# Kernel optimization log

Measured on AMD Instinct MI355X. Metric: run time of the kernel, lower is better.

## Reference

```python
import jax, jax.numpy as jnp
import numpy as np

NUM_HEADS = 16

def _stablemax3_s(x):
    # 3rd-order Taylor approx of exp(x), Eq 38
    pos = 1.0 + x * (1.0 + 0.5 * x * (1.0 + x / 3.0))
    neg = 1.0 / (1.0 - x * (1.0 - 0.5 * x * (1.0 - x / 3.0)))
    return jnp.where(x >= 0, pos, neg)

def stablemax3(logits, axis=-1):
    logits = logits - jnp.max(logits, axis=axis, keepdims=True)
    s = _stablemax3_s(logits)
    return s / jnp.sum(s, axis=axis, keepdims=True)

def setup_inputs() -> dict:
    key = jax.random.key(0)
    k1, k2, k3 = jax.random.split(key, 3)
    B, S, D = 2, 2048, 1024
    x = jax.random.normal(k1, (B, S, D), dtype=jnp.float32)
    w_qkv = jax.random.normal(k2, (3 * D, D), dtype=jnp.float32) * 0.02
    w_out = jax.random.normal(k3, (D, D), dtype=jnp.float32) * 0.02
    b_out = jnp.zeros((D,), dtype=jnp.float32)
    return {"x": x, "w_qkv": w_qkv, "w_out": w_out, "b_out": b_out}

def reference(x, w_qkv, w_out, b_out):
    B, S, D = x.shape
    H = NUM_HEADS
    hd = D // H
    scale = hd ** (-0.5)
    qkv = x @ w_qkv.T                                  # [B, S, 3D]
    qkv = qkv.reshape(B, S, 3, H, hd)
    qkv = jnp.transpose(qkv, (2, 0, 3, 1, 4))          # [3, B, H, S, hd]
    q, k, v = qkv[0], qkv[1], qkv[2]                   # pos(.) is identity here
    attn = jnp.einsum('bhsd,bhtd->bhst', q, k) * scale # [B, H, S, S]
    attn = stablemax3(attn, axis=-1)
    out = jnp.einsum('bhst,bhtd->bhsd', attn, v)       # [B, H, S, hd]
    out = jnp.transpose(out, (0, 2, 1, 3)).reshape(B, S, D)
    return out @ w_out.T + b_out
```

## Files before the change

### kernel.cpp

```cpp
#include <hip/hip_runtime.h>

typedef _Float16 half8 __attribute__((ext_vector_type(8)));
typedef _Float16 half4 __attribute__((ext_vector_type(4)));
typedef float floatx4 __attribute__((ext_vector_type(4)));

__device__ __forceinline__ void gl_lds16(const _Float16* g, _Float16* l) {
    __builtin_amdgcn_global_load_lds(
        (const __attribute__((address_space(1))) void*)g,
        (__attribute__((address_space(3))) void*)l, 16, 0, 0);
}

__global__ __launch_bounds__(256) void cvt_f32_f16(const floatx4* __restrict__ in,
                                                   half4* __restrict__ out, int n4) {
    int i = blockIdx.x * 256 + threadIdx.x;
    if (i >= n4) return;
    floatx4 v = in[i];
    half4 h;
#pragma unroll
    for (int j = 0; j < 4; ++j) h[j] = (_Float16)v[j];
    out[i] = h;
}

__global__ __launch_bounds__(256) void gemm_qkv(const _Float16* __restrict__ A,
                                                const _Float16* __restrict__ B,
                                                _Float16* __restrict__ qh,
                                                _Float16* __restrict__ kh,
                                                _Float16* __restrict__ vth) {
    const int K = 1024;
    __shared__ _Float16 SH[128 * 68];
    _Float16* As = SH;
    _Float16* Bs = SH + 4096;
    const int t = threadIdx.x;
    const int lane = t & 63, w = t >> 6;
    const int l15 = lane & 15, quad = lane >> 4;
    const int wm = w >> 1, wn = w & 1;
    const int m0 = blockIdx.y * 128, n0 = blockIdx.x * 128;

    floatx4 acc[4][4];
    const floatx4 zf = {0.f, 0.f, 0.f, 0.f};
#pragma unroll
    for (int i = 0; i < 4; ++i)
#pragma unroll
        for (int j = 0; j < 4; ++j) acc[i][j] = zf;

    for (int kt = 0; kt < K; kt += 32) {
        __syncthreads();
#pragma unroll
        for (int it = 0; it < 2; ++it) {
            int cc = it * 256 + t;
            int row = cc >> 2, kc = cc & 3;
            gl_lds16(&A[(size_t)(m0 + row) * K + kt + kc * 8], &As[cc * 8]);
            gl_lds16(&B[(size_t)(n0 + row) * K + kt + kc * 8], &Bs[cc * 8]);
        }
        __syncthreads();
        half8 af[4], bfr[4];
#pragma unroll
        for (int i = 0; i < 4; ++i)
            af[i] = *(const half8*)&As[(wm * 64 + i * 16 + l15) * 32 + quad * 8];
#pragma unroll
        for (int i = 0; i < 4; ++i)
            bfr[i] = *(const half8*)&Bs[(wn * 64 + i * 16 + l15) * 32 + quad * 8];
#pragma unroll
        for (int mi = 0; mi < 4; ++mi)
#pragma unroll
            for (int ni = 0; ni < 4; ++ni)
                acc[mi][ni] = __builtin_amdgcn_mfma_f32_16x16x32_f16(af[mi], bfr[ni],
                                                                     acc[mi][ni], 0, 0, 0);
    }

    const int b = m0 >> 11, s0 = m0 & 2047;
#pragma unroll
    for (int hf = 0; hf < 2; ++hf) {
        __syncthreads();
        if (wn == hf) {
#pragma unroll
            for (int mi = 0; mi < 4; ++mi)
#pragma unroll
                for (int ni = 0; ni < 4; ++ni)
#pragma unroll
                    for (int r = 0; r < 4; ++r)
                        SH[(wm * 64 + mi * 16 + quad * 4 + r) * 68 + ni * 16 + l15] =
                            (_Float16)acc[mi][ni][r];
        }
        __syncthreads();
        const int cbase = n0 + hf * 64;
        if (n0 < 2048) {
            const int hh = (cbase & 1023) >> 6;
            _Float16* dst = (n0 < 1024 ? qh : kh) + (size_t)((b << 4) | hh) * 131072;
#pragma unroll
            for (int it = 0; it < 4; ++it) {
                int cc = it * 256 + t;
                int r = cc >> 3, c8 = cc & 7;
                half4 lo = *(const half4*)&SH[r * 68 + c8 * 8];
                half4 hi = *(const half4*)&SH[r * 68 + c8 * 8 + 4];
                half8 v;
#pragma unroll
                for (int j = 0; j < 4; ++j) { v[j] = lo[j]; v[j + 4] = hi[j]; }
                *(half8*)&dst[(size_t)(s0 + r) * 64 + c8 * 8] = v;
            }
        } else {
            const int hh = (cbase - 2048) >> 6;
            _Float16* dst = vth + (size_t)((b << 4) | hh) * 131072;
#pragma unroll
            for (int it = 0; it < 4; ++it) {
                int cc = it * 256 + t;
                int d = cc >> 4, s8 = cc & 15;
                half8 v;
#pragma unroll
                for (int j = 0; j < 8; ++j) v[j] = SH[(s8 * 8 + j) * 68 + d];
                *(half8*)&dst[(size_t)d * 2048 + s0 + s8 * 8] = v;
            }
        }
    }
}

__global__ __launch_bounds__(256) void gemm_out(const _Float16* __restrict__ A,
                                                const _Float16* __restrict__ B,
                                                float* __restrict__ C,
                                                const float* __restrict__ bias) {
    const int K = 1024, N = 1024;
    __shared__ _Float16 SH[6144];
    _Float16* As = SH;
    _Float16* Bs = SH + 2048;
    const int t = threadIdx.x;
    const int lane = t & 63, w = t >> 6;
    const int l15 = lane & 15, quad = lane >> 4;
    const int wm = w >> 1, wn = w & 1;
    const int m0 = blockIdx.y * 64, n0 = blockIdx.x * 128;

    floatx4 acc[2][4];
    const floatx4 zf = {0.f, 0.f, 0.f, 0.f};
#pragma unroll
    for (int i = 0; i < 2; ++i)
#pragma unroll
        for (int j = 0; j < 4; ++j) acc[i][j] = zf;

    for (int kt = 0; kt < K; kt += 32) {
        __syncthreads();
        {
            int row = t >> 2, kc = t & 3;
            gl_lds16(&A[(size_t)(m0 + row) * K + kt + kc * 8], &As[t * 8]);
        }
#pragma unroll
        for (int it = 0; it < 2; ++it) {
            int cc = it * 256 + t;
            int row = cc >> 2, kc = cc & 3;
            gl_lds16(&B[(size_t)(n0 + row) * K + kt + kc * 8], &Bs[cc * 8]);
        }
        __syncthreads();
        half8 af[2], bfr[4];
#pragma unroll
        for (int i = 0; i < 2; ++i)
            af[i] = *(const half8*)&As[(wm * 32 + i * 16 + l15) * 32 + quad * 8];
#pragma unroll
        for (int i = 0; i < 4; ++i)
            bfr[i] = *(const half8*)&Bs[(wn * 64 + i * 16 + l15) * 32 + quad * 8];
#pragma unroll
        for (int mi = 0; mi < 2; ++mi)
#pragma unroll
            for (int ni = 0; ni < 4; ++ni)
                acc[mi][ni] = __builtin_amdgcn_mfma_f32_16x16x32_f16(af[mi], bfr[ni],
                                                                     acc[mi][ni], 0, 0, 0);
    }

#pragma unroll
    for (int mi = 0; mi < 2; ++mi) {
#pragma unroll
        for (int ni = 0; ni < 4; ++ni) {
            int col = n0 + wn * 64 + ni * 16 + l15;
            float bv = bias[col];
#pragma unroll
            for (int r = 0; r < 4; ++r) {
                int row = m0 + wm * 32 + mi * 16 + quad * 4 + r;
                C[(size_t)row * N + col] = acc[mi][ni][r] + bv;
            }
        }
    }
}

__device__ inline float s3pos(float a) {
    float h = fmaf(a, 0.16666667f, 0.5f);
    h = fmaf(a, h, 1.0f);
    return fmaf(a, h, 1.0f);
}

__global__ __launch_bounds__(256) void attn_kernel(const _Float16* __restrict__ qh,
                                                   const _Float16* __restrict__ kh,
                                                   const _Float16* __restrict__ vth,
                                                   _Float16* __restrict__ out) {
    __shared__ _Float16 SM[2 * 64 * 72];
    _Float16* Ks = SM;
    _Float16* VTs = SM + 64 * 72;

    const int t = threadIdx.x;
    const int lane = t & 63, w = t >> 6;
    const int l15 = lane & 15, quad = lane >> 4;
    const int q0 = blockIdx.x * 128;
    const int bh = blockIdx.y;
    const int b = bh >> 4, h = bh & 15;

    const _Float16* Qp = qh + (size_t)bh * 131072 + q0 * 64;
    const _Float16* Kp = kh + (size_t)bh * 131072;
    const _Float16* VTp = vth + (size_t)bh * 131072;

    const floatx4 zf = {0.f, 0.f, 0.f, 0.f};

    half8 qf[2][2];
#pragma unroll
    for (int nh = 0; nh < 2; ++nh)
#pragma unroll
        for (int kk = 0; kk < 2; ++kk)
            qf[nh][kk] = *(const half8*)&Qp[(w * 32 + nh * 16 + l15) * 64 + kk * 32 + quad * 8];

    float rmax[2] = {-1.0e30f, -1.0e30f};

    for (int kt = 0; kt < 2048; kt += 64) {
        __syncthreads();
#pragma unroll
        for (int it = 0; it < 2; ++it) {
            int cc = it * 256 + t;
            int r = cc >> 3, c8 = cc & 7;
            *(half8*)&Ks[r * 72 + c8 * 8] = *(const half8*)&Kp[kt * 64 + cc * 8];
        }
        __syncthreads();
        floatx4 sa[4][2];
#pragma unroll
        for (int T = 0; T < 4; ++T) { sa[T][0] = zf; sa[T][1] = zf; }
#pragma unroll
        for (int kk = 0; kk < 2; ++kk) {
            half8 kf[4];
#pragma unroll
            for (int T = 0; T < 4; ++T)
                kf[T] = *(const half8*)&Ks[(T * 16 + l15) * 72 + kk * 32 + quad * 8];
#pragma unroll
            for (int T = 0; T < 4; ++T)
#pragma unroll
                for (int nh = 0; nh < 2; ++nh)
                    sa[T][nh] = __builtin_amdgcn_mfma_f32_16x16x32_f16(kf[T], qf[nh][kk],
                                                                      sa[T][nh], 0, 0, 0);
        }
#pragma unroll
        for (int T = 0; T < 4; ++T)
#pragma unroll
            for (int nh = 0; nh < 2; ++nh)
#pragma unroll
                for (int r = 0; r < 4; ++r)
                    rmax[nh] = fmaxf(rmax[nh], sa[T][nh][r]);
    }
#pragma unroll
    for (int nh = 0; nh < 2; ++nh) {
        rmax[nh] = fmaxf(rmax[nh], __shfl_xor(rmax[nh], 16, 64));
        rmax[nh] = fmaxf(rmax[nh], __shfl_xor(rmax[nh], 32, 64));
    }
    const float xm[2] = {-0.125f * rmax[0], -0.125f * rmax[1]};

    float rsum[2] = {0.f, 0.f};
    floatx4 oacc[4][2];
#pragma unroll
    for (int i = 0; i < 4; ++i) { oacc[i][0] = zf; oacc[i][1] = zf; }

    for (int kt = 0; kt < 2048; kt += 64) {
        __syncthreads();
#pragma unroll
        for (int it = 0; it < 2; ++it) {
            int cc = it * 256 + t;
            int r = cc >> 3, c8 = cc & 7;
            *(half8*)&Ks[r * 72 + c8 * 8] = *(const half8*)&Kp[kt * 64 + cc * 8];
            *(half8*)&VTs[r * 72 + c8 * 8] =
                *(const half8*)&VTp[(size_t)r * 2048 + kt + c8 * 8];
        }
        __syncthreads();
        floatx4 sa[4][2];
#pragma unroll
        for (int T = 0; T < 4; ++T) { sa[T][0] = zf; sa[T][1] = zf; }
#pragma unroll
        for (int kk = 0; kk < 2; ++kk) {
            half8 kf[4];
#pragma unroll
            for (int T = 0; T < 4; ++T)
                kf[T] = *(const half8*)&Ks[(T * 16 + l15) * 72 + kk * 32 + quad * 8];
#pragma unroll
            for (int T = 0; T < 4; ++T)
#pragma unroll
                for (int nh = 0; nh < 2; ++nh)
                    sa[T][nh] = __builtin_amdgcn_mfma_f32_16x16x32_f16(kf[T], qf[nh][kk],
                                                                      sa[T][nh], 0, 0, 0);
        }
        float p[2][4][4];
#pragma unroll
        for (int nh = 0; nh < 2; ++nh)
#pragma unroll
            for (int T = 0; T < 4; ++T)
#pragma unroll
                for (int r = 0; r < 4; ++r) {
                    float x = fmaf(sa[T][nh][r], 0.125f, xm[nh]);
                    float pv = __builtin_amdgcn_rcpf(s3pos(fabsf(x)));
                    p[nh][T][r] = pv;
                    rsum[nh] += pv;
                }
#pragma unroll
        for (int c = 0; c < 2; ++c) {
            half8 vf[4];
#pragma unroll
            for (int di = 0; di < 4; ++di) {
                half4 lo = *(const half4*)&VTs[(di * 16 + l15) * 72 + c * 32 + 4 * quad];
                half4 hi = *(const half4*)&VTs[(di * 16 + l15) * 72 + c * 32 + 16 + 4 * quad];
                half8 vv;
#pragma unroll
                for (int j = 0; j < 4; ++j) { vv[j] = lo[j]; vv[j + 4] = hi[j]; }
                vf[di] = vv;
            }
#pragma unroll
            for (int nh = 0; nh < 2; ++nh) {
                half8 pb;
#pragma unroll
                for (int j = 0; j < 8; ++j)
                    pb[j] = (_Float16)p[nh][2 * c + (j >> 2)][j & 3];
#pragma unroll
                for (int di = 0; di < 4; ++di)
                    oacc[di][nh] = __builtin_amdgcn_mfma_f32_16x16x32_f16(vf[di], pb,
                                                                         oacc[di][nh], 0, 0, 0);
            }
        }
    }

#pragma unroll
    for (int nh = 0; nh < 2; ++nh) {
        rsum[nh] += __shfl_xor(rsum[nh], 16, 64);
        rsum[nh] += __shfl_xor(rsum[nh], 32, 64);
    }
    const float inv[2] = {1.0f / rsum[0], 1.0f / rsum[1]};

    __syncthreads();
    _Float16* Os = SM;
#pragma unroll
    for (int di = 0; di < 4; ++di) {
#pragma unroll
        for (int nh = 0; nh < 2; ++nh) {
            half4 hv;
#pragma unroll
            for (int r = 0; r < 4; ++r) hv[r] = (_Float16)(oacc[di][nh][r] * inv[nh]);
            *(half4*)&Os[(w * 32 + nh * 16 + l15) * 72 + di * 16 + quad * 4] = hv;
        }
    }
    __syncthreads();
    _Float16* Op = out + (size_t)(b * 2048 + q0) * 1024 + h * 64;
#pragma unroll
    for (int it = 0; it < 4; ++it) {
        int cc = it * 256 + t;
        int r = cc >> 3, c8 = cc & 7;
        *(half8*)&Op[(size_t)r * 1024 + c8 * 8] = *(const half8*)&Os[r * 72 + c8 * 8];
    }
}

extern "C" void kernel_launch(void* const* d_in, const int* in_sizes, int n_in,
                              void* d_out, int out_size, void* d_ws, size_t ws_size,
                              hipStream_t stream) {
    const float* x_f = (const float*)d_in[0];
    const float* wqkv_f = (const float*)d_in[1];
    const float* wout_f = (const float*)d_in[2];
    const float* bias_f = (const float*)d_in[3];

    char* ws = (char*)d_ws;
    _Float16* xh = (_Float16*)(ws);
    _Float16* aoh = xh;
    _Float16* wqh = (_Float16*)(ws + 8388608);
    _Float16* woh = wqh;
    _Float16* qh = (_Float16*)(ws + 14680064);
    _Float16* kh = (_Float16*)(ws + 23068672);
    _Float16* vth = (_Float16*)(ws + 31457280);

    cvt_f32_f16<<<4096, 256, 0, stream>>>((const floatx4*)x_f, (half4*)xh, 1048576);
    cvt_f32_f16<<<3072, 256, 0, stream>>>((const floatx4*)wqkv_f, (half4*)wqh, 786432);
    gemm_qkv<<<dim3(24, 32), 256, 0, stream>>>(xh, wqh, qh, kh, vth);
    cvt_f32_f16<<<1024, 256, 0, stream>>>((const floatx4*)wout_f, (half4*)woh, 262144);
    attn_kernel<<<dim3(16, 32), 256, 0, stream>>>(qh, kh, vth, aoh);
    gemm_out<<<dim3(8, 64), 256, 0, stream>>>(aoh, woh, (float*)d_out, bias_f);
}
```

Baseline: 218.3 us.

## Double K-tile depth in GEMMs and attention, fuse input conversion kernels

New measurement: 259.2 us. +18.7%, slower.

```diff
diff --git a/kernel.cpp b/kernel.cpp
--- a/kernel.cpp
+++ b/kernel.cpp
@@ -8,6 +8,27 @@
     __builtin_amdgcn_global_load_lds(
         (const __attribute__((address_space(1))) void*)g,
         (__attribute__((address_space(3))) void*)l, 16, 0, 0);
+}
+
+__global__ __launch_bounds__(256) void cvt_xw(const floatx4* __restrict__ x,
+                                              const floatx4* __restrict__ wq,
+                                              half4* __restrict__ xh,
+                                              half4* __restrict__ wqh) {
+    int i = blockIdx.x * 256 + threadIdx.x;
+    floatx4 v;
+    half4 h;
+    if (i < 1048576) {
+        v = x[i];
+#pragma unroll
+        for (int j = 0; j < 4; ++j) h[j] = (_Float16)v[j];
+        xh[i] = h;
+    } else {
+        int j4 = i - 1048576;
+        v = wq[j4];
+#pragma unroll
+        for (int j = 0; j < 4; ++j) h[j] = (_Float16)v[j];
+        wqh[j4] = h;
+    }
 }
 
 __global__ __launch_bounds__(256) void cvt_f32_f16(const floatx4* __restrict__ in,
@@ -27,140 +48,148 @@
                                                 _Float16* __restrict__ kh,
                                                 _Float16* __restrict__ vth) {
     const int K = 1024;
-    __shared__ _Float16 SH[128 * 68];
+    __shared__ _Float16 SH[128 * 128];
+    _Float16* As = SH;
+    _Float16* Bs = SH + 8192;
+    const int t = threadIdx.x;
+    const int lane = t & 63, w = t >> 6;
+    const int l15 = lane & 15, quad = lane >> 4;
+    const int wm = w >> 1, wn = w & 1;
+    const int m0 = blockIdx.y * 128, n0 = blockIdx.x * 128;
+
+    floatx4 acc[4][4];
+    const floatx4 zf = {0.f, 0.f, 0.f, 0.f};
+#pragma unroll
+    for (int i = 0; i < 4; ++i)
+#pragma unroll
+        for (int j = 0; j < 4; ++j) acc[i][j] = zf;
+
+    for (int kt = 0; kt < K; kt += 64) {
+        __syncthreads();
+#pragma unroll
+        for (int it = 0; it < 4; ++it) {
+            int cc = it * 256 + t;
+            int row = cc >> 3, kc = cc & 7;
+            gl_lds16(&A[(size_t)(m0 + row) * K + kt + kc * 8], &As[cc * 8]);
+            gl_lds16(&B[(size_t)(n0 + row) * K + kt + kc * 8], &Bs[cc * 8]);
+        }
+        __syncthreads();
+#pragma unroll
+        for (int kk = 0; kk < 2; ++kk) {
+            half8 af[4], bfr[4];
+#pragma unroll
+            for (int i = 0; i < 4; ++i)
+                af[i] = *(const half8*)&As[(wm * 64 + i * 16 + l15) * 64 + kk * 32 + quad * 8];
+#pragma unroll
+            for (int i = 0; i < 4; ++i)
+                bfr[i] = *(const half8*)&Bs[(wn * 64 + i * 16 + l15) * 64 + kk * 32 + quad * 8];
+#pragma unroll
+            for (int mi = 0; mi < 4; ++mi)
+#pragma unroll
+                for (int ni = 0; ni < 4; ++ni)
+                    acc[mi][ni] = __builtin_amdgcn_mfma_f32_16x16x32_f16(af[mi], bfr[ni],
+                                                                         acc[mi][ni], 0, 0, 0);
+        }
+    }
+
+    const int b = m0 >> 11, s0 = m0 & 2047;
+#pragma unroll
+    for (int hf = 0; hf < 2; ++hf) {
+        __syncthreads();
+        if (wn == hf) {
+#pragma unroll
+            for (int mi = 0; mi < 4; ++mi)
+#pragma unroll
+                for (int ni = 0; ni < 4; ++ni)
+#pragma unroll
+                    for (int r = 0; r < 4; ++r)
+                        SH[(wm * 64 + mi * 16 + quad * 4 + r) * 68 + ni * 16 + l15] =
+                            (_Float16)acc[mi][ni][r];
+        }
+        __syncthreads();
+        const int cbase = n0 + hf * 64;
+        if (n0 < 2048) {
+            const int hh = (cbase & 1023) >> 6;
+            _Float16* dst = (n0 < 1024 ? qh : kh) + (size_t)((b << 4) | hh) * 131072;
+#pragma unroll
+            for (int it = 0; it < 4; ++it) {
+                int cc = it * 256 + t;
+                int r = cc >> 3, c8 = cc & 7;
+                half4 lo = *(const half4*)&SH[r * 68 + c8 * 8];
+                half4 hi = *(const half4*)&SH[r * 68 + c8 * 8 + 4];
+                half8 v;
+#pragma unroll
+                for (int j = 0; j < 4; ++j) { v[j] = lo[j]; v[j + 4] = hi[j]; }
+                *(half8*)&dst[(size_t)(s0 + r) * 64 + c8 * 8] = v;
+            }
+        } else {
+            const int hh = (cbase - 2048) >> 6;
+            _Float16* dst = vth + (size_t)((b << 4) | hh) * 131072;
+#pragma unroll
+            for (int it = 0; it < 4; ++it) {
+                int cc = it * 256 + t;
+                int d = cc >> 4, s8 = cc & 15;
+                half8 v;
+#pragma unroll
+                for (int j = 0; j < 8; ++j) v[j] = SH[(s8 * 8 + j) * 68 + d];
+                *(half8*)&dst[(size_t)d * 2048 + s0 + s8 * 8] = v;
+            }
+        }
+    }
+}
+
+__global__ __launch_bounds__(256) void gemm_out(const _Float16* __restrict__ A,
+                                                const _Float16* __restrict__ B,
+                                                float* __restrict__ C,
+                                                const float* __restrict__ bias) {
+    const int K = 1024, N = 1024;
+    __shared__ _Float16 SH[12288];
     _Float16* As = SH;
     _Float16* Bs = SH + 4096;
     const int t = threadIdx.x;
     const int lane = t & 63, w = t >> 6;
     const int l15 = lane & 15, quad = lane >> 4;
     const int wm = w >> 1, wn = w & 1;
-    const int m0 = blockIdx.y * 128, n0 = blockIdx.x * 128;
-
-    floatx4 acc[4][4];
+    const int m0 = blockIdx.y * 64, n0 = blockIdx.x * 128;
+
+    floatx4 acc[2][4];
     const floatx4 zf = {0.f, 0.f, 0.f, 0.f};
 #pragma unroll
-    for (int i = 0; i < 4; ++i)
+    for (int i = 0; i < 2; ++i)
 #pragma unroll
         for (int j = 0; j < 4; ++j) acc[i][j] = zf;
 
-    for (int kt = 0; kt < K; kt += 32) {
+    for (int kt = 0; kt < K; kt += 64) {
         __syncthreads();
 #pragma unroll
         for (int it = 0; it < 2; ++it) {
             int cc = it * 256 + t;
-            int row = cc >> 2, kc = cc & 3;
+            int row = cc >> 3, kc = cc & 7;
             gl_lds16(&A[(size_t)(m0 + row) * K + kt + kc * 8], &As[cc * 8]);
+        }
+#pragma unroll
+        for (int it = 0; it < 4; ++it) {
+            int cc = it * 256 + t;
+            int row = cc >> 3, kc = cc & 7;
             gl_lds16(&B[(size_t)(n0 + row) * K + kt + kc * 8], &Bs[cc * 8]);
         }
         __syncthreads();
-        half8 af[4], bfr[4];
-#pragma unroll
-        for (int i = 0; i < 4; ++i)
-            af[i] = *(const half8*)&As[(wm * 64 + i * 16 + l15) * 32 + quad * 8];
-#pragma unroll
-        for (int i = 0; i < 4; ++i)
-            bfr[i] = *(const half8*)&Bs[(wn * 64 + i * 16 + l15) * 32 + quad * 8];
-#pragma unroll
-        for (int mi = 0; mi < 4; ++mi)
-#pragma unroll
-            for (int ni = 0; ni < 4; ++ni)
-                acc[mi][ni] = __builtin_amdgcn_mfma_f32_16x16x32_f16(af[mi], bfr[ni],
-                                                                     acc[mi][ni], 0, 0, 0);
-    }
-
-    const int b = m0 >> 11, s0 = m0 & 2047;
-#pragma unroll
-    for (int hf = 0; hf < 2; ++hf) {
-        __syncthreads();
-        if (wn == hf) {
-#pragma unroll
-            for (int mi = 0; mi < 4; ++mi)
+#pragma unroll
+        for (int kk = 0; kk < 2; ++kk) {
+            half8 af[2], bfr[4];
+#pragma unroll
+            for (int i = 0; i < 2; ++i)
+                af[i] = *(const half8*)&As[(wm * 32 + i * 16 + l15) * 64 + kk * 32 + quad * 8];
+#pragma unroll
+            for (int i = 0; i < 4; ++i)
+                bfr[i] = *(const half8*)&Bs[(wn * 64 + i * 16 + l15) * 64 + kk * 32 + quad * 8];
+#pragma unroll
+            for (int mi = 0; mi < 2; ++mi)
 #pragma unroll
                 for (int ni = 0; ni < 4; ++ni)
-#pragma unroll
-                    for (int r = 0; r < 4; ++r)
-                        SH[(wm * 64 + mi * 16 + quad * 4 + r) * 68 + ni * 16 + l15] =
-                            (_Float16)acc[mi][ni][r];
-        }
-        __syncthreads();
-        const int cbase = n0 + hf * 64;
-        if (n0 < 2048) {
-            const int hh = (cbase & 1023) >> 6;
-            _Float16* dst = (n0 < 1024 ? qh : kh) + (size_t)((b << 4) | hh) * 131072;
-#pragma unroll
-            for (int it = 0; it < 4; ++it) {
-                int cc = it * 256 + t;
-                int r = cc >> 3, c8 = cc & 7;
-                half4 lo = *(const half4*)&SH[r * 68 + c8 * 8];
-                half4 hi = *(const half4*)&SH[r * 68 + c8 * 8 + 4];
-                half8 v;
-#pragma unroll
-                for (int j = 0; j < 4; ++j) { v[j] = lo[j]; v[j + 4] = hi[j]; }
-                *(half8*)&dst[(size_t)(s0 + r) * 64 + c8 * 8] = v;
-            }
-        } else {
-            const int hh = (cbase - 2048) >> 6;
-            _Float16* dst = vth + (size_t)((b << 4) | hh) * 131072;
-#pragma unroll
-            for (int it = 0; it < 4; ++it) {
-                int cc = it * 256 + t;
-                int d = cc >> 4, s8 = cc & 15;
-                half8 v;
-#pragma unroll
-                for (int j = 0; j < 8; ++j) v[j] = SH[(s8 * 8 + j) * 68 + d];
-                *(half8*)&dst[(size_t)d * 2048 + s0 + s8 * 8] = v;
-            }
-        }
-    }
-}
-
-__global__ __launch_bounds__(256) void gemm_out(const _Float16* __restrict__ A,
-                                                const _Float16* __restrict__ B,
-                                                float* __restrict__ C,
-                                                const float* __restrict__ bias) {
-    const int K = 1024, N = 1024;
-    __shared__ _Float16 SH[6144];
-    _Float16* As = SH;
-    _Float16* Bs = SH + 2048;
-    const int t = threadIdx.x;
-    const int lane = t & 63, w = t >> 6;
-    const int l15 = lane & 15, quad = lane >> 4;
-    const int wm = w >> 1, wn = w & 1;
-    const int m0 = blockIdx.y * 64, n0 = blockIdx.x * 128;
-
-    floatx4 acc[2][4];
-    const floatx4 zf = {0.f, 0.f, 0.f, 0.f};
-#pragma unroll
-    for (int i = 0; i < 2; ++i)
-#pragma unroll
-        for (int j = 0; j < 4; ++j) acc[i][j] = zf;
-
-    for (int kt = 0; kt < K; kt += 32) {
-        __syncthreads();
-        {
-            int row = t >> 2, kc = t & 3;
-            gl_lds16(&A[(size_t)(m0 + row) * K + kt + kc * 8], &As[t * 8]);
-        }
-#pragma unroll
-        for (int it = 0; it < 2; ++it) {
-            int cc = it * 256 + t;
-            int row = cc >> 2, kc = cc & 3;
-            gl_lds16(&B[(size_t)(n0 + row) * K + kt + kc * 8], &Bs[cc * 8]);
-        }
-        __syncthreads();
-        half8 af[2], bfr[4];
-#pragma unroll
-        for (int i = 0; i < 2; ++i)
-            af[i] = *(const half8*)&As[(wm * 32 + i * 16 + l15) * 32 + quad * 8];
-#pragma unroll
-        for (int i = 0; i < 4; ++i)
-            bfr[i] = *(const half8*)&Bs[(wn * 64 + i * 16 + l15) * 32 + quad * 8];
-#pragma unroll
-        for (int mi = 0; mi < 2; ++mi)
-#pragma unroll
-            for (int ni = 0; ni < 4; ++ni)
-                acc[mi][ni] = __builtin_amdgcn_mfma_f32_16x16x32_f16(af[mi], bfr[ni],
-                                                                     acc[mi][ni], 0, 0, 0);
+                    acc[mi][ni] = __builtin_amdgcn_mfma_f32_16x16x32_f16(af[mi], bfr[ni],
+                                                                         acc[mi][ni], 0, 0, 0);
+        }
     }
 
 #pragma unroll
@@ -188,9 +217,8 @@
                                                    const _Float16* __restrict__ kh,
                                                    const _Float16* __restrict__ vth,
                                                    _Float16* __restrict__ out) {
-    __shared__ _Float16 SM[2 * 64 * 72];
-    _Float16* Ks = SM;
-    _Float16* VTs = SM + 64 * 72;
+    __shared__ _Float16 Ks[128 * 72];
+    __shared__ _Float16 VTs[64 * 136];
 
     const int t = threadIdx.x;
     const int lane = t & 63, w = t >> 6;
@@ -214,33 +242,33 @@
 
     float rmax[2] = {-1.0e30f, -1.0e30f};
 
-    for (int kt = 0; kt < 2048; kt += 64) {
-        __syncthreads();
-#pragma unroll
-        for (int it = 0; it < 2; ++it) {
+    for (int kt = 0; kt < 2048; kt += 128) {
+        __syncthreads();
+#pragma unroll
+        for (int it = 0; it < 4; ++it) {
             int cc = it * 256 + t;
             int r = cc >> 3, c8 = cc & 7;
-            *(half8*)&Ks[r * 72 + c8 * 8] = *(const half8*)&Kp[kt * 64 + cc * 8];
-        }
-        __syncthreads();
-        floatx4 sa[4][2];
-#pragma unroll
-        for (int T = 0; T < 4; ++T) { sa[T][0] = zf; sa[T][1] = zf; }
+            *(half8*)&Ks[r * 72 + c8 * 8] = *(const half8*)&Kp[(size_t)(kt + r) * 64 + c8 * 8];
+        }
+        __syncthreads();
+        floatx4 sa[8][2];
+#pragma unroll
+        for (int T = 0; T < 8; ++T) { sa[T][0] = zf; sa[T][1] = zf; }
 #pragma unroll
         for (int kk = 0; kk < 2; ++kk) {
-            half8 kf[4];
-#pragma unroll
-            for (int T = 0; T < 4; ++T)
+            half8 kf[8];
+#pragma unroll
+            for (int T = 0; T < 8; ++T)
                 kf[T] = *(const half8*)&Ks[(T * 16 + l15) * 72 + kk * 32 + quad * 8];
 #pragma unroll
-            for (int T = 0; T < 4; ++T)
+            for (int T = 0; T < 8; ++T)
 #pragma unroll
                 for (int nh = 0; nh < 2; ++nh)
                     sa[T][nh] = __builtin_amdgcn_mfma_f32_16x16x32_f16(kf[T], qf[nh][kk],
                                                                       sa[T][nh], 0, 0, 0);
         }
 #pragma unroll
-        for (int T = 0; T < 4; ++T)
+        for (int T = 0; T < 8; ++T)
 #pragma unroll
             for (int nh = 0; nh < 2; ++nh)
 #pragma unroll
@@ -259,52 +287,41 @@
 #pragma unroll
     for (int i = 0; i < 4; ++i) { oacc[i][0] = zf; oacc[i][1] = zf; }
 
-    for (int kt = 0; kt < 2048; kt += 64) {
-        __syncthreads();
-#pragma unroll
-        for (int it = 0; it < 2; ++it) {
+    for (int kt = 0; kt < 2048; kt += 128) {
+        __syncthreads();
+#pragma unroll
+        for (int it = 0; it < 4; ++it) {
             int cc = it * 256 + t;
             int r = cc >> 3, c8 = cc & 7;
-            *(half8*)&Ks[r * 72 + c8 * 8] = *(const half8*)&Kp[kt * 64 + cc * 8];
-            *(half8*)&VTs[r * 72 + c8 * 8] =
-                *(const half8*)&VTp[(size_t)r * 2048 + kt + c8 * 8];
-        }
-        __syncthreads();
-        floatx4 sa[4][2];
-#pragma unroll
-        for (int T = 0; T < 4; ++T) { sa[T][0] = zf; sa[T][1] = zf; }
+            *(half8*)&Ks[r * 72 + c8 * 8] = *(const half8*)&Kp[(size_t)(kt + r) * 64 + c8 * 8];
+            int d = cc >> 4, k8 = cc & 15;
+            *(half8*)&VTs[d * 136 + k8 * 8] =
+                *(const half8*)&VTp[(size_t)d * 2048 + kt + k8 * 8];
+        }
+        __syncthreads();
+        floatx4 sa[8][2];
+#pragma unroll
+        for (int T = 0; T < 8; ++T) { sa[T][0] = zf; sa[T][1] = zf; }
 #pragma unroll
         for (int kk = 0; kk < 2; ++kk) {
-            half8 kf[4];
-#pragma unroll
-            for (int T = 0; T < 4; ++T)
+            half8 kf[8];
+#pragma unroll
+            for (int T = 0; T < 8; ++T)
                 kf[T] = *(const half8*)&Ks[(T * 16 + l15) * 72 + kk * 32 + quad * 8];
 #pragma unroll
-            for (int T = 0; T < 4; ++T)
+            for (int T = 0; T < 8; ++T)
 #pragma unroll
                 for (int nh = 0; nh < 2; ++nh)
                     sa[T][nh] = __builtin_amdgcn_mfma_f32_16x16x32_f16(kf[T], qf[nh][kk],
                                                                       sa[T][nh], 0, 0, 0);
         }
-        float p[2][4][4];
-#pragma unroll
-        for (int nh = 0; nh < 2; ++nh)
-#pragma unroll
-            for (int T = 0; T < 4; ++T)
-#pragma unroll
-                for (int r = 0; r < 4; ++r) {
-                    float x = fmaf(sa[T][nh][r], 0.125f, xm[nh]);
-                    float pv = __builtin_amdgcn_rcpf(s3pos(fabsf(x)));
-                    p[nh][T][r] = pv;
-                    rsum[nh] += pv;
-                }
-#pragma unroll
-        for (int c = 0; c < 2; ++c) {
+#pragma unroll
+        for (int c = 0; c < 4; ++c) {
             half8 vf[4];
 #pragma unroll
             for (int di = 0; di < 4; ++di) {
-                half4 lo = *(const half4*)&VTs[(di * 16 + l15) * 72 + c * 32 + 4 * quad];
-                half4 hi = *(const half4*)&VTs[(di * 16 + l15) * 72 + c * 32 + 16 + 4 * quad];
+                half4 lo = *(const half4*)&VTs[(di * 16 + l15) * 136 + c * 32 + 4 * quad];
+                half4 hi = *(const half4*)&VTs[(di * 16 + l15) * 136 + c * 32 + 16 + 4 * quad];
                 half8 vv;
 #pragma unroll
                 for (int j = 0; j < 4; ++j) { vv[j] = lo[j]; vv[j + 4] = hi[j]; }
@@ -314,8 +331,12 @@
             for (int nh = 0; nh < 2; ++nh) {
                 half8 pb;
 #pragma unroll
-                for (int j = 0; j < 8; ++j)
-                    pb[j] = (_Float16)p[nh][2 * c + (j >> 2)][j & 3];
+                for (int j = 0; j < 8; ++j) {
+                    float x = fmaf(sa[2 * c + (j >> 2)][nh][j & 3], 0.125f, xm[nh]);
+                    float pv = __builtin_amdgcn_rcpf(s3pos(fabsf(x)));
+                    rsum[nh] += pv;
+                    pb[j] = (_Float16)pv;
+                }
 #pragma unroll
                 for (int di = 0; di < 4; ++di)
                     oacc[di][nh] = __builtin_amdgcn_mfma_f32_16x16x32_f16(vf[di], pb,
@@ -332,7 +353,7 @@
     const float inv[2] = {1.0f / rsum[0], 1.0f / rsum[1]};
 
     __syncthreads();
-    _Float16* Os = SM;
+    _Float16* Os = Ks;
 #pragma unroll
     for (int di = 0; di < 4; ++di) {
 #pragma unroll
@@ -370,8 +391,8 @@
     _Float16* kh = (_Float16*)(ws + 23068672);
     _Float16* vth = (_Float16*)(ws + 31457280);
 
-    cvt_f32_f16<<<4096, 256, 0, stream>>>((const floatx4*)x_f, (half4*)xh, 1048576);
-    cvt_f32_f16<<<3072, 256, 0, stream>>>((const floatx4*)wqkv_f, (half4*)wqh, 786432);
+    cvt_xw<<<7168, 256, 0, stream>>>((const floatx4*)x_f, (const floatx4*)wqkv_f,
+                                     (half4*)xh, (half4*)wqh);
     gemm_qkv<<<dim3(24, 32), 256, 0, stream>>>(xh, wqh, qh, kh, vth);
     cvt_f32_f16<<<1024, 256, 0, stream>>>((const floatx4*)wout_f, (half4*)woh, 262144);
     attn_kernel<<<dim3(16, 32), 256, 0, stream>>>(qh, kh, vth, aoh);
```
